# Kernel optimization log

Hardware: AMD Instinct MI355X
Metric: run time of the kernel (lower is better)

Reference implementation:

```python
import jax, jax.numpy as jnp
import numpy as np

V = 255      # v_size
L = 16       # l_size = e_size // v_size (row/col weight of cyclic H)
E = V * L    # e_size
P = 8        # num_permu
B = 1024     # batch
CLIP = 10.0


def _build_indices():
    # Synthetic cyclic H: H[i, j] = 1 iff (j - i) % V in S, |S| = L.
    # Reproduces the torch precompute: pos_cyclic_col / pos_cyclic_row edge
    # orderings and the two edge-permutations between them, plus the
    # num_permu codeword permutations (perma).
    rng = np.random.default_rng(0)
    S = np.sort(rng.choice(V, size=L, replace=False))
    U = S                                  # sorted column offsets per row
    T = np.sort((-S) % V)                  # sorted row offsets per column
    m = np.searchsorted(U, (-T) % V)       # row-ordering slot of each col-slot
    C = np.arange(V)[:, None]
    K = np.arange(L)[None, :]
    R = (T[None, :] + C) % V               # row of k-th edge in column c
    idx_c = (C * L + K).ravel()            # edge index in cyclic-col ordering
    idx_r = (R * L + m[None, :]).ravel()   # same edge in cyclic-row ordering
    rc = np.empty(E, np.int32); rc[idx_c] = idx_r   # cycrowtocyccol
    cr = np.empty(E, np.int32); cr[idx_r] = idx_c   # cyccoltocycrow
    perma = np.stack([rng.permutation(V + 1) for _ in range(P)]).astype(np.int32)
    return rc, cr, perma


def setup_inputs() -> dict:
    key = jax.random.key(0)
    ks = jax.random.split(key, 4)
    rc, cr, perma = _build_indices()
    return {
        "x": jax.random.normal(ks[0], (B, V + 1), jnp.float32),
        "message": jnp.zeros((B, P * E), jnp.float32),
        "oddw_v": jax.random.normal(ks[1], (5, L), jnp.float32),
        "oddw_e": jax.random.normal(ks[2], (5, L, L), jnp.float32),
        "w_e_out": jax.random.normal(ks[3], (L,), jnp.float32),
        "perma": jnp.asarray(perma),
        "rc_idx": jnp.asarray(rc),
        "cr_idx": jnp.asarray(cr),
    }


def reference(x, message, oddw_v, oddw_e, w_e_out, perma, rc_idx, cr_idx):
    Bx = x.shape[0]
    dt = x.dtype
    mask_e = 1.0 - jnp.eye(L, dtype=dt)    # zero diagonal (extrinsic mask)
    idx_v = perma[:, 1:]                   # [P, V]: permute rows, drop row 0

    def odd_layer(ev, wv, we):
        # ev: edge messages [B, P, V, L] in cyclic-col edge ordering
        v0 = x[:, :, None] * wv                                  # [B, V+1, L]
        v_out = v0[:, idx_v, :]                                  # [B, P, V, L]
        e = ev.reshape(Bx, P, E)[:, :, rc_idx].reshape(Bx, P, V, L)
        e_intra = jnp.einsum('bpvl,lm->bpvm', e, we * mask_e)
        return jnp.tanh(0.5 * jnp.clip(v_out + e_intra, -CLIP, CLIP))

    def even_layer(o, flag_clip):
        e = o.reshape(Bx, P, E)[:, :, cr_idx].reshape(Bx, P, V, L)
        e = e + (jnp.abs(e) == 0).astype(dt)            # zeros -> 1
        r = jnp.prod(e, axis=-1, keepdims=True) / e     # leave-one-out product
        if flag_clip:
            r = jnp.clip(r, -CLIP, CLIP)
        return jnp.log((1.0 + r) / (1.0 - r + 1e-9) + 1e-9)

    ev = message.reshape(Bx, P, V, L)
    for t in range(5):                     # 5 BP iterations (fixed depth)
        ev = even_layer(odd_layer(ev, oddw_v[t], oddw_e[t]), t == 0)

    # output layer
    e = ev.reshape(Bx, P, E)[:, :, rc_idx].reshape(Bx, P, V, L)
    eo = jnp.einsum('bpvl,l->bpv', e, w_e_out)          # [B, P, V]
    eo = jnp.pad(eo, ((0, 0), (0, 0), (1, 0)))          # zero at position 0
    idx = jnp.broadcast_to(perma[None].astype(jnp.int32), eo.shape)
    total = jnp.take_along_axis(eo, idx, axis=2).sum(axis=1)  # [B, V+1]
    return x + total
```

## Files before the change

### kernel.cpp

```cpp
#include <hip/hip_runtime.h>

#define V 255
#define VS 256
#define L 16
#define P 8
#define CLIPV 10.0f

typedef __attribute__((ext_vector_type(2))) float f32x2;

__device__ __forceinline__ f32x2 splat(float a) { return (f32x2){a, a}; }
__device__ __forceinline__ f32x2 pk_fma(f32x2 a, f32x2 b, f32x2 c) {
    return __builtin_elementwise_fma(a, b, c);
}

__device__ __forceinline__ f32x2 tanh_half_clip_pk(f32x2 s) {
    f32x2 t = __builtin_elementwise_min(
                  __builtin_elementwise_max(s, splat(-CLIPV)), splat(CLIPV));
    f32x2 r;
    float ex = __expf(t.x); r.x = 1.0f - __fdividef(2.0f, ex + 1.0f);
    float ey = __expf(t.y); r.y = 1.0f - __fdividef(2.0f, ey + 1.0f);
    return r;
}

__device__ __forceinline__ f32x2 zsub(f32x2 o) {
    o.x = (o.x == 0.0f) ? 1.0f : o.x;
    o.y = (o.y == 0.0f) ? 1.0f : o.y;
    return o;
}

template <int MODE>
__global__ __launch_bounds__(256, 4) void bpd_kernel(
    const float* __restrict__ x,
    const float* __restrict__ oddw_v,
    const float* __restrict__ oddw_e,
    const float* __restrict__ w_e_out,
    const int*   __restrict__ perma,
    const int*   __restrict__ rc_idx,
    const int*   __restrict__ cr_idx,
    float* __restrict__ eo_ws,
    const int* __restrict__ invp,
    float* __restrict__ out)
{
    __shared__ f32x2 OO[L * VS];
    __shared__ f32x2 TOT[VS];

    const int tid = threadIdx.x;
    const int blk = blockIdx.x;
    const int b  = blk >> 2;
    const int pA = (blk & 3) * 2;
    const int pB = pA + 1;
    const int v  = tid;
    const int vi = (v < V) ? v : (V - 1);

    f32x2 xv;
    {
        const float* xrow = x + b * (V + 1);
        const int vc = (v < V) ? (v + 1) : V;
        xv.x = xrow[perma[pA * (V + 1) + vc]];
        xv.y = xrow[perma[pB * (V + 1) + vc]];
    }

    int offc[L];
    int offt[L];
    {
        const int4* rc4 = (const int4*)(rc_idx + vi * L);
        const int4* cr4 = (const int4*)(cr_idx + vi * L);
#pragma unroll
        for (int i = 0; i < 4; ++i) {
            int4 a = rc4[i];
            int4 c = cr4[i];
            offc[4*i+0] = ((c.x & 15) << 8) | (c.x >> 4);
            offc[4*i+1] = ((c.y & 15) << 8) | (c.y >> 4);
            offc[4*i+2] = ((c.z & 15) << 8) | (c.z >> 4);
            offc[4*i+3] = ((c.w & 15) << 8) | (c.w >> 4);
            offt[4*i+0] = a.x >> 4;
            offt[4*i+1] = a.y >> 4;
            offt[4*i+2] = a.z >> 4;
            offt[4*i+3] = a.w >> 4;
        }
    }

    f32x2 ev[L];
#pragma unroll
    for (int m = 0; m < L; ++m)
        ev[m] = zsub(tanh_half_clip_pk(xv * oddw_v[m]));

#pragma unroll
    for (int t = 0; t < 5; ++t) {
#pragma unroll
        for (int m = 0; m < L; ++m) OO[(m << 8) + v] = ev[m];
        __syncthreads();

        {
            f32x2 t0 = OO[offc[0]],  t1 = OO[offc[1]];
            f32x2 t2 = OO[offc[2]],  t3 = OO[offc[3]];
#pragma unroll
            for (int l = 4; l < L; l += 4) {
                t0 = t0 * OO[offc[l + 0]];
                t1 = t1 * OO[offc[l + 1]];
                t2 = t2 * OO[offc[l + 2]];
                t3 = t3 * OO[offc[l + 3]];
            }
            TOT[v] = (t0 * t1) * (t2 * t3);
        }
        __syncthreads();

#pragma unroll
        for (int l = 0; l < L; ++l) {
            f32x2 Tl = TOT[offt[l]];
            f32x2 e  = ev[l];
            f32x2 num = e + Tl;
            f32x2 den = pk_fma(e, splat(1e-9f), e - Tl);
            f32x2 o;
            o.x = __logf(__fdividef(num.x, den.x));
            o.y = __logf(__fdividef(num.y, den.y));
            ev[l] = o;
        }

        if (t < 4) {
            const float* __restrict__ wv = oddw_v + (t + 1) * L;
            const float* __restrict__ wm = oddw_e + (t + 1) * (L * L);
            f32x2 s[L];
#pragma unroll
            for (int m = 0; m < L; ++m) s[m] = xv * wv[m];
#pragma unroll
            for (int l = 0; l < L; ++l) {
                const f32x2 el = ev[l];
#pragma unroll
                for (int m = 0; m < L; ++m) {
                    if (m != l)
                        s[m] = pk_fma(el, splat(wm[l * L + m]), s[m]);
                }
            }
#pragma unroll
            for (int m = 0; m < L; ++m)
                ev[m] = zsub(tanh_half_clip_pk(s[m]));
        }
    }

    {
        f32x2 d = splat(0.0f);
#pragma unroll
        for (int l = 0; l < L; ++l)
            d = pk_fma(ev[l], splat(w_e_out[l]), d);
        if (v < V) {
            const int uA = blk * 2;
            if (MODE == 0) {
                eo_ws[(size_t)uA * V + v]       = d.x;
                eo_ws[(size_t)(uA + 1) * V + v] = d.y;
            } else {
                int ja = invp[pA * (V + 1) + (v + 1)];
                int jb = invp[pB * (V + 1) + (v + 1)];
                atomicAdd(&out[b * (V + 1) + ja], d.x);
                atomicAdd(&out[b * (V + 1) + jb], d.y);
            }
        }
    }
}

__global__ __launch_bounds__(256) void out_kernel(
    const float* __restrict__ x,
    const float* __restrict__ eo_ws,
    const int* __restrict__ perma,
    float* __restrict__ out)
{
    const int b = blockIdx.x;
    const int j = threadIdx.x;
    float acc = x[b * (V + 1) + j];
#pragma unroll
    for (int p = 0; p < P; ++p) {
        int idx = perma[p * (V + 1) + j];
        if (idx > 0) acc += eo_ws[((size_t)(b * P + p)) * V + (idx - 1)];
    }
    out[b * (V + 1) + j] = acc;
}

__global__ __launch_bounds__(256) void inv_kernel(const int* __restrict__ perma,
                                                  int* __restrict__ invp)
{
    int p = blockIdx.x, j = threadIdx.x;
    invp[p * (V + 1) + perma[p * (V + 1) + j]] = j;
}

__global__ __launch_bounds__(256) void copy_kernel(const float* __restrict__ x,
                                                   float* __restrict__ out, int n)
{
    int i = blockIdx.x * 256 + threadIdx.x;
    if (i < n) out[i] = x[i];
}

extern "C" void kernel_launch(void* const* d_in, const int* in_sizes, int n_in,
                              void* d_out, int out_size, void* d_ws, size_t ws_size,
                              hipStream_t stream)
{
    const float* x       = (const float*)d_in[0];
    const float* oddw_v  = (const float*)d_in[2];
    const float* oddw_e  = (const float*)d_in[3];
    const float* w_e_out = (const float*)d_in[4];
    const int*   perma   = (const int*)d_in[5];
    const int*   rc      = (const int*)d_in[6];
    const int*   cr      = (const int*)d_in[7];
    float* out = (float*)d_out;

    const int Bx = in_sizes[0] / (V + 1);
    const int nunits = Bx * P;
    const int npairs = nunits / 2;
    const size_t need = (size_t)nunits * V * sizeof(float);

    if (ws_size >= need) {
        float* eo = (float*)d_ws;
        hipLaunchKernelGGL((bpd_kernel<0>), dim3(npairs), dim3(256), 0, stream,
                           x, oddw_v, oddw_e, w_e_out, perma, rc, cr,
                           eo, (const int*)nullptr, (float*)nullptr);
        hipLaunchKernelGGL(out_kernel, dim3(Bx), dim3(256), 0, stream,
                           x, eo, perma, out);
    } else {
        int* invp = (int*)d_ws;
        hipLaunchKernelGGL(inv_kernel, dim3(P), dim3(V + 1), 0, stream, perma, invp);
        hipLaunchKernelGGL(copy_kernel, dim3((out_size + 255) / 256), dim3(256), 0, stream,
                           x, out, out_size);
        hipLaunchKernelGGL((bpd_kernel<1>), dim3(npairs), dim3(256), 0, stream,
                           x, oddw_v, oddw_e, w_e_out, perma, rc, cr,
                           (float*)nullptr, invp, out);
    }
}
```

Measured before the change: 234.1 us.

## Compute intra-edge 16x16 mixing with fp16 MFMA instead of scalar packed FMAs

The per-vertex 16x16 odd-layer matrix multiply, previously done with packed fp32 FMAs in registers, now runs on MFMA f16 16x16x16 instructions. Edge messages are staged in LDS as half precision, and the tanh results are written straight back into the shared OO buffer. OO and TOT get a 257 stride to reduce bank conflicts, the gather offsets are packed into one register each, and the outer loop is no longer unrolled, with launch bounds relaxed to 2 waves per EU. This cuts VALU work and register pressure, but it adds LDS traffic, extra barriers and fp16 rounding of messages and weights, which can change accuracy.

```diff
diff --git a/kernel.cpp b/kernel.cpp
--- a/kernel.cpp
+++ b/kernel.cpp
@@ -1,35 +1,32 @@
 #include <hip/hip_runtime.h>
 
 #define V 255
-#define VS 256
 #define L 16
 #define P 8
 #define CLIPV 10.0f
 
 typedef __attribute__((ext_vector_type(2))) float f32x2;
+typedef __attribute__((ext_vector_type(4))) float floatx4;
+typedef __attribute__((ext_vector_type(4))) _Float16 half4;
 
 __device__ __forceinline__ f32x2 splat(float a) { return (f32x2){a, a}; }
 __device__ __forceinline__ f32x2 pk_fma(f32x2 a, f32x2 b, f32x2 c) {
     return __builtin_elementwise_fma(a, b, c);
 }
-
-__device__ __forceinline__ f32x2 tanh_half_clip_pk(f32x2 s) {
-    f32x2 t = __builtin_elementwise_min(
-                  __builtin_elementwise_max(s, splat(-CLIPV)), splat(CLIPV));
-    f32x2 r;
-    float ex = __expf(t.x); r.x = 1.0f - __fdividef(2.0f, ex + 1.0f);
-    float ey = __expf(t.y); r.y = 1.0f - __fdividef(2.0f, ey + 1.0f);
-    return r;
-}
-
-__device__ __forceinline__ f32x2 zsub(f32x2 o) {
-    o.x = (o.x == 0.0f) ? 1.0f : o.x;
-    o.y = (o.y == 0.0f) ? 1.0f : o.y;
-    return o;
+__device__ __forceinline__ unsigned pkh2(float a, float b) {
+    _Float16 ha = (_Float16)a, hb = (_Float16)b;
+    return (unsigned)__builtin_bit_cast(unsigned short, ha) |
+           ((unsigned)__builtin_bit_cast(unsigned short, hb) << 16);
+}
+__device__ __forceinline__ float tanh_zsub(float s) {
+    float t = fminf(fmaxf(s, -CLIPV), CLIPV);
+    float e = __expf(t);
+    float o = 1.0f - __fdividef(2.0f, e + 1.0f);
+    return (o == 0.0f) ? 1.0f : o;
 }
 
 template <int MODE>
-__global__ __launch_bounds__(256, 4) void bpd_kernel(
+__global__ __launch_bounds__(256, 2) void bmf_kernel(
     const float* __restrict__ x,
     const float* __restrict__ oddw_v,
     const float* __restrict__ oddw_e,
@@ -41,8 +38,10 @@
     const int* __restrict__ invp,
     float* __restrict__ out)
 {
-    __shared__ f32x2 OO[L * VS];
-    __shared__ f32x2 TOT[VS];
+    __shared__ f32x2 OO[L * 257];
+    __shared__ f32x2 TOT[257];
+    __shared__ f32x2 XG[256];
+    __shared__ __align__(16) unsigned A_lds[512 * 10];
 
     const int tid = threadIdx.x;
     const int blk = blockIdx.x;
@@ -51,17 +50,22 @@
     const int pB = pA + 1;
     const int v  = tid;
     const int vi = (v < V) ? v : (V - 1);
+    const int vc = (v < V) ? (v + 1) : V;
+
+    const int lane = tid & 63;
+    const int wid  = tid >> 6;
+    const int c16  = lane & 15;
+    const int g    = lane >> 4;
 
     f32x2 xv;
     {
         const float* xrow = x + b * (V + 1);
-        const int vc = (v < V) ? (v + 1) : V;
         xv.x = xrow[perma[pA * (V + 1) + vc]];
         xv.y = xrow[perma[pB * (V + 1) + vc]];
     }
-
-    int offc[L];
-    int offt[L];
+    XG[v] = xv;
+
+    unsigned pk[L];
     {
         const int4* rc4 = (const int4*)(rc_idx + vi * L);
         const int4* cr4 = (const int4*)(cr_idx + vi * L);
@@ -69,37 +73,36 @@
         for (int i = 0; i < 4; ++i) {
             int4 a = rc4[i];
             int4 c = cr4[i];
-            offc[4*i+0] = ((c.x & 15) << 8) | (c.x >> 4);
-            offc[4*i+1] = ((c.y & 15) << 8) | (c.y >> 4);
-            offc[4*i+2] = ((c.z & 15) << 8) | (c.z >> 4);
-            offc[4*i+3] = ((c.w & 15) << 8) | (c.w >> 4);
-            offt[4*i+0] = a.x >> 4;
-            offt[4*i+1] = a.y >> 4;
-            offt[4*i+2] = a.z >> 4;
-            offt[4*i+3] = a.w >> 4;
-        }
+            pk[4*i+0] = ((unsigned)(a.x >> 4) << 16) | ((c.x & 15) * 257 + (c.x >> 4));
+            pk[4*i+1] = ((unsigned)(a.y >> 4) << 16) | ((c.y & 15) * 257 + (c.y >> 4));
+            pk[4*i+2] = ((unsigned)(a.z >> 4) << 16) | ((c.z & 15) * 257 + (c.z >> 4));
+            pk[4*i+3] = ((unsigned)(a.w >> 4) << 16) | ((c.w & 15) * 257 + (c.w >> 4));
+        }
+    }
+
+#pragma unroll
+    for (int m = 0; m < L; ++m) {
+        float w0 = oddw_v[m];
+        f32x2 e;
+        e.x = tanh_zsub(xv.x * w0);
+        e.y = tanh_zsub(xv.y * w0);
+        OO[m * 257 + v] = e;
     }
 
     f32x2 ev[L];
-#pragma unroll
-    for (int m = 0; m < L; ++m)
-        ev[m] = zsub(tanh_half_clip_pk(xv * oddw_v[m]));
-
-#pragma unroll
+#pragma unroll 1
     for (int t = 0; t < 5; ++t) {
-#pragma unroll
-        for (int m = 0; m < L; ++m) OO[(m << 8) + v] = ev[m];
         __syncthreads();
 
         {
-            f32x2 t0 = OO[offc[0]],  t1 = OO[offc[1]];
-            f32x2 t2 = OO[offc[2]],  t3 = OO[offc[3]];
+            f32x2 t0 = OO[pk[0] & 0xffffu], t1 = OO[pk[1] & 0xffffu];
+            f32x2 t2 = OO[pk[2] & 0xffffu], t3 = OO[pk[3] & 0xffffu];
 #pragma unroll
             for (int l = 4; l < L; l += 4) {
-                t0 = t0 * OO[offc[l + 0]];
-                t1 = t1 * OO[offc[l + 1]];
-                t2 = t2 * OO[offc[l + 2]];
-                t3 = t3 * OO[offc[l + 3]];
+                t0 = t0 * OO[pk[l + 0] & 0xffffu];
+                t1 = t1 * OO[pk[l + 1] & 0xffffu];
+                t2 = t2 * OO[pk[l + 2] & 0xffffu];
+                t3 = t3 * OO[pk[l + 3] & 0xffffu];
             }
             TOT[v] = (t0 * t1) * (t2 * t3);
         }
@@ -107,8 +110,8 @@
 
 #pragma unroll
         for (int l = 0; l < L; ++l) {
-            f32x2 Tl = TOT[offt[l]];
-            f32x2 e  = ev[l];
+            f32x2 e  = OO[l * 257 + v];
+            f32x2 Tl = TOT[pk[l] >> 16];
             f32x2 num = e + Tl;
             f32x2 den = pk_fma(e, splat(1e-9f), e - Tl);
             f32x2 o;
@@ -117,43 +120,76 @@
             ev[l] = o;
         }
 
-        if (t < 4) {
-            const float* __restrict__ wv = oddw_v + (t + 1) * L;
-            const float* __restrict__ wm = oddw_e + (t + 1) * (L * L);
-            f32x2 s[L];
-#pragma unroll
-            for (int m = 0; m < L; ++m) s[m] = xv * wv[m];
-#pragma unroll
-            for (int l = 0; l < L; ++l) {
-                const f32x2 el = ev[l];
-#pragma unroll
-                for (int m = 0; m < L; ++m) {
-                    if (m != l)
-                        s[m] = pk_fma(el, splat(wm[l * L + m]), s[m]);
+        if (t == 4) break;
+
+#pragma unroll
+        for (int u = 0; u < 2; ++u) {
+            unsigned* dst = &A_lds[(u * 256 + v) * 10];
+            unsigned aw[8];
+#pragma unroll
+            for (int q = 0; q < 8; ++q)
+                aw[q] = pkh2(ev[2 * q][u], ev[2 * q + 1][u]);
+#pragma unroll
+            for (int q = 0; q < 4; ++q)
+                *(uint2*)(dst + 2 * q) = (uint2){aw[2 * q], aw[2 * q + 1]};
+        }
+        __syncthreads();
+
+        {
+            const float* __restrict__ wmn = oddw_e + (t + 1) * (L * L);
+            half4 bfrag;
+#pragma unroll
+            for (int j = 0; j < 4; ++j) {
+                int k = 4 * g + j;
+                float w = wmn[k * L + c16];
+                if (k == c16) w = 0.0f;
+                bfrag[j] = (_Float16)w;
+            }
+            const float wvv = oddw_v[(t + 1) * L + c16];
+
+            const int rowbase = wid * 64;
+#pragma unroll
+            for (int tt = 0; tt < 4; ++tt) {
+                const int rb = rowbase + tt * 16;
+                f32x2 xg0 = XG[rb + 4 * g + 0];
+                f32x2 xg1 = XG[rb + 4 * g + 1];
+                f32x2 xg2 = XG[rb + 4 * g + 2];
+                f32x2 xg3 = XG[rb + 4 * g + 3];
+#pragma unroll
+                for (int u = 0; u < 2; ++u) {
+                    uint2 ar = *(const uint2*)
+                        &A_lds[(u * 256 + rb + c16) * 10 + g * 2];
+                    floatx4 cb;
+                    cb[0] = xg0[u] * wvv;
+                    cb[1] = xg1[u] * wvv;
+                    cb[2] = xg2[u] * wvv;
+                    cb[3] = xg3[u] * wvv;
+                    floatx4 d = __builtin_amdgcn_mfma_f32_16x16x16f16(
+                        __builtin_bit_cast(half4, ar), bfrag, cb, 0, 0, 0);
+#pragma unroll
+                    for (int j = 0; j < 4; ++j) {
+                        float e = tanh_zsub(d[j]);
+                        ((float*)OO)[(c16 * 257 + (rb + 4 * g + j)) * 2 + u] = e;
+                    }
                 }
             }
-#pragma unroll
-            for (int m = 0; m < L; ++m)
-                ev[m] = zsub(tanh_half_clip_pk(s[m]));
-        }
-    }
-
-    {
+        }
+    }
+
+    if (v < V) {
         f32x2 d = splat(0.0f);
 #pragma unroll
         for (int l = 0; l < L; ++l)
             d = pk_fma(ev[l], splat(w_e_out[l]), d);
-        if (v < V) {
-            const int uA = blk * 2;
-            if (MODE == 0) {
-                eo_ws[(size_t)uA * V + v]       = d.x;
-                eo_ws[(size_t)(uA + 1) * V + v] = d.y;
-            } else {
-                int ja = invp[pA * (V + 1) + (v + 1)];
-                int jb = invp[pB * (V + 1) + (v + 1)];
-                atomicAdd(&out[b * (V + 1) + ja], d.x);
-                atomicAdd(&out[b * (V + 1) + jb], d.y);
-            }
+        const int uA = blk * 2;
+        if (MODE == 0) {
+            eo_ws[(size_t)uA * V + v]       = d.x;
+            eo_ws[(size_t)(uA + 1) * V + v] = d.y;
+        } else {
+            int ja = invp[pA * (V + 1) + (v + 1)];
+            int jb = invp[pB * (V + 1) + (v + 1)];
+            atomicAdd(&out[b * (V + 1) + ja], d.x);
+            atomicAdd(&out[b * (V + 1) + jb], d.y);
         }
     }
 }
@@ -209,7 +245,7 @@
 
     if (ws_size >= need) {
         float* eo = (float*)d_ws;
-        hipLaunchKernelGGL((bpd_kernel<0>), dim3(npairs), dim3(256), 0, stream,
+        hipLaunchKernelGGL((bmf_kernel<0>), dim3(npairs), dim3(256), 0, stream,
                            x, oddw_v, oddw_e, w_e_out, perma, rc, cr,
                            eo, (const int*)nullptr, (float*)nullptr);
         hipLaunchKernelGGL(out_kernel, dim3(Bx), dim3(256), 0, stream,
@@ -219,7 +255,7 @@
         hipLaunchKernelGGL(inv_kernel, dim3(P), dim3(V + 1), 0, stream, perma, invp);
         hipLaunchKernelGGL(copy_kernel, dim3((out_size + 255) / 256), dim3(256), 0, stream,
                            x, out, out_size);
-        hipLaunchKernelGGL((bpd_kernel<1>), dim3(npairs), dim3(256), 0, stream,
+        hipLaunchKernelGGL((bmf_kernel<1>), dim3(npairs), dim3(256), 0, stream,
                            x, oddw_v, oddw_e, w_e_out, perma, rc, cr,
                            (float*)nullptr, invp, out);
     }
```

Result: no change. 235.2 us (+0.5%).
